# Performance work log

Hardware: AMD Instinct MI355X
Metric: run time of the kernel (lower is better)

The kernel has to match this reference:

```python
import jax, jax.numpy as jnp
import numpy as np

SCALE = 2
GROUPS = 4


def _init_pos(scale, groups, dtype=jnp.float32):
    # h = arange((-s+1)/2, (s-1)/2 + 1) / s
    h = (jnp.arange(scale, dtype=dtype) - (scale - 1) / 2) / scale
    yy, xx = jnp.meshgrid(h, h, indexing='ij')
    pos = jnp.stack([xx, yy], axis=0)              # [2, s, s]
    # torch .repeat(1, groups, 1, 1) tiles along the size-2 dim -> [2*G, s, s]
    return jnp.tile(pos, (groups, 1, 1)).reshape(1, -1, 1, 1)  # [1, 2*G*s*s, 1, 1]


def _pixel_shuffle(x, r):
    B, C, H, W = x.shape
    Co = C // (r * r)
    x = x.reshape(B, Co, r, r, H, W)
    x = x.transpose(0, 1, 4, 2, 5, 3)              # [B, Co, H, r, W, r]
    return x.reshape(B, Co, H * r, W * r)


def _grid_sample_border(img, grid):
    # img: [N, C, H, W]; grid: [N, Ho, Wo, 2] in [-1, 1] (x, y); bilinear,
    # align_corners=False, padding_mode='border' (coords clamped first).
    N, C, H, W = img.shape
    gx, gy = grid[..., 0], grid[..., 1]
    ix = jnp.clip(((gx + 1) * W - 1) * 0.5, 0.0, W - 1)
    iy = jnp.clip(((gy + 1) * H - 1) * 0.5, 0.0, H - 1)
    x0f = jnp.floor(ix); y0f = jnp.floor(iy)
    wx = (ix - x0f)[:, None]                       # [N, 1, Ho, Wo]
    wy = (iy - y0f)[:, None]
    x0 = x0f.astype(jnp.int32); y0 = y0f.astype(jnp.int32)
    x1 = jnp.minimum(x0 + 1, W - 1); y1 = jnp.minimum(y0 + 1, H - 1)

    def gather(im, y, x):                          # im [C,H,W], y/x [Ho,Wo]
        return im[:, y, x]                         # [C, Ho, Wo]
    gv = jax.vmap(gather)

    return ((1 - wy) * ((1 - wx) * gv(img, y0, x0) + wx * gv(img, y0, x1))
            + wy * ((1 - wx) * gv(img, y1, x0) + wx * gv(img, y1, x1)))


def setup_inputs() -> dict:
    key = jax.random.key(0)
    k1, k2 = jax.random.split(key)
    B, C, H, W = 16, 64, 128, 128
    out_ch = 2 * GROUPS * SCALE ** 2               # 32
    x = jax.random.normal(k1, (B, C, H, W), dtype=jnp.float32)
    w_off = jax.random.normal(k2, (out_ch, C), dtype=jnp.float32) * 0.001
    b_off = jnp.zeros((out_ch,), dtype=jnp.float32)
    return {"x": x, "w_off": w_off, "b_off": b_off}


def reference(x, w_off, b_off):
    B, C, H, W = x.shape
    s, G = SCALE, GROUPS
    # 1x1 conv offset, scaled by 0.25, plus fixed sub-pixel init positions
    offset = jnp.einsum('bchw,oc->bohw', x, w_off) + b_off[None, :, None, None]
    offset = offset * 0.25 + _init_pos(s, G, x.dtype)   # [B, 2*G*s*s, H, W]

    off = offset.reshape(B, 2, G * s * s, H, W)
    cx = jnp.arange(W, dtype=x.dtype) + 0.5
    cy = jnp.arange(H, dtype=x.dtype) + 0.5
    yy, xx = jnp.meshgrid(cy, cx, indexing='ij')
    coords = jnp.stack([xx, yy], axis=0)[None, :, None]  # [1, 2, 1, H, W]
    norm = jnp.array([W, H], dtype=x.dtype).reshape(1, 2, 1, 1, 1)
    coords = 2 * (coords + off) / norm - 1               # [B, 2, G*s*s, H, W]

    coords = _pixel_shuffle(coords.reshape(B, 2 * G * s * s, H, W), s)  # [B, 2G, sH, sW]
    grid = coords.reshape(B, 2, G, s * H, s * W)
    grid = grid.transpose(0, 2, 3, 4, 1).reshape(B * G, s * H, s * W, 2)

    out = _grid_sample_border(x.reshape(B * G, C // G, H, W), grid)
    return out.reshape(B, C, s * H, s * W)
```

## Files before the change

### kernel.cpp

```cpp
#include <hip/hip_runtime.h>
#include <hip/hip_fp16.h>


namespace {
constexpr int CC = 64;
constexpr int HH = 128;
constexpr int WW = 128;
constexpr int HW = HH * WW;
constexpr int OW = 2 * WW;
constexpr int OHW = 4 * HW;
constexpr int TH = 8, TW = 32;
constexpr int WS = 36;
constexpr int WPL = 10 * WS;
constexpr int RING = 84;
typedef float vfloat2 __attribute__((ext_vector_type(2)));
}

__global__ __launch_bounds__(256, 2)
void dysample_kernel(const float* __restrict__ x,
                     const float* __restrict__ w_off,
                     const float* __restrict__ b_off,
                     float* __restrict__ out) {
    __shared__ float win[16][WPL];

    const int tid  = threadIdx.x;
    const int wg   = ((int)blockIdx.x & 7) * 128 + ((int)blockIdx.x >> 3);
    const int tile = wg & 63;
    const int b    = wg >> 6;
    const int th0  = (tile >> 2) * TH;
    const int tw0  = (tile & 3) * TW;
    const int ty   = tid >> 5;
    const int tx   = tid & 31;
    const int h    = th0 + ty;
    const int w    = tw0 + tx;

    float xv[64];
    __half2 offs[16];
    {
        float accx[16], accy[16];
#pragma unroll
        for (int j = 0; j < 16; ++j) {
            accx[j] = b_off[j];
            accy[j] = b_off[j + 16];
        }
        const float* xb = x + b * (CC * HW) + h * WW + w;
#pragma unroll
        for (int ch = 0; ch < 4; ++ch) {
#pragma unroll
            for (int c = 0; c < 16; ++c) xv[ch * 16 + c] = xb[(ch * 16 + c) * HW];
#pragma unroll
            for (int j = 0; j < 16; ++j) {
                float ax = accx[j], ay = accy[j];
                const float* wxp = w_off + j * 64 + ch * 16;
                const float* wyp = wxp + 16 * 64;
#pragma unroll
                for (int c = 0; c < 16; ++c) ax = fmaf(xv[ch * 16 + c], wxp[c], ax);
#pragma unroll
                for (int c = 0; c < 16; ++c) ay = fmaf(xv[ch * 16 + c], wyp[c], ay);
                accx[j] = ax; accy[j] = ay;
            }
        }
#pragma unroll
        for (int j = 0; j < 16; ++j) {
            const int g = j >> 2, r1_ = (j >> 1) & 1, r2_ = j & 1;
            const float init = (((g & 1) ? r1_ : r2_) ? 0.25f : -0.25f);
            offs[j] = __floats2half2_rn(fmaf(accx[j], 0.25f, init),
                                        fmaf(accy[j], 0.25f, init));
        }
    }

    int rsrc[6], rdst[6];
#pragma unroll
    for (int i = 0; i < 6; ++i) {
        const int s  = tid + 256 * i;
        const int ci = min(s / RING, 15);
        const int rp = s - ci * RING;
        int ry, rx;
        if (rp < 34)      { ry = 0;       rx = rp; }
        else if (rp < 68) { ry = 9;       rx = rp - 34; }
        else if (rp < 76) { ry = rp - 67; rx = 0; }
        else              { ry = rp - 75; rx = 33; }
        const int gr = min(max(th0 - 1 + ry, 0), HH - 1);
        const int gc = min(max(tw0 - 1 + rx, 0), WW - 1);
        rsrc[i] = ci * HW + gr * WW + gc;
        rdst[i] = ci * WPL + ry * WS + rx;
    }
    const bool v5 = (tid < 16 * RING - 5 * 256);

    const float* xg0 = x + (size_t)b * (CC * HW);
    float ringv[6];
#pragma unroll
    for (int i = 0; i < 6; ++i)
        if (i < 5 || v5) ringv[i] = xg0[rsrc[i]];

    float* const ob = out + (size_t)b * (CC * OHW)
                    + (size_t)(2 * h) * OW + 2 * w;
    const float fw = (float)w, fh = (float)h;

#pragma unroll
    for (int g = 0; g < 4; ++g) {
        __syncthreads();
#pragma unroll
        for (int ci = 0; ci < 16; ++ci)
            win[ci][(ty + 1) * WS + (tx + 1)] = xv[g * 16 + ci];
#pragma unroll
        for (int i = 0; i < 6; ++i)
            if (i < 5 || v5) (&win[0][0])[rdst[i]] = ringv[i];
        __syncthreads();
        if (g < 3) {
#pragma unroll
            for (int i = 0; i < 6; ++i)
                if (i < 5 || v5) ringv[i] = xg0[(g + 1) * (16 * HW) + rsrc[i]];
        }

        float wc[4][3], wr[4][3];
        bool vall = true;
#pragma unroll
        for (int p = 0; p < 4; ++p) {
            const float2 o = __half22float2(offs[g * 4 + p]);
            float ix = ((fw + 0.5f) + o.x) - 0.5f;
            float iy = ((fh + 0.5f) + o.y) - 0.5f;
            ix = fminf(fmaxf(ix, 0.0f), 127.0f);
            iy = fminf(fmaxf(iy, 0.0f), 127.0f);
            const float x0f = floorf(ix), y0f = floorf(iy);
            const float wxf = ix - x0f, wyf = iy - y0f;
            const int sx = (int)x0f - (w - 1);
            const int sy = (int)y0f - (h - 1);
            vall = vall && ((unsigned)sx <= 1u) && ((unsigned)sy <= 1u);
            const bool bx = (sx != 0), by = (sy != 0);
            wc[p][0] = bx ? 0.0f : 1.0f - wxf;
            wc[p][1] = bx ? 1.0f - wxf : wxf;
            wc[p][2] = bx ? wxf : 0.0f;
            wr[p][0] = by ? 0.0f : 1.0f - wyf;
            wr[p][1] = by ? 1.0f - wyf : wyf;
            wr[p][2] = by ? wyf : 0.0f;
        }

        float* const og = ob + (size_t)(g * 16) * OHW;
        if (vall) {
#pragma unroll 2
            for (int c = 0; c < 16; ++c) {
                const float* wp = &win[c][ty * WS + tx];
                const float m0 = wp[0],        m1 = wp[1],          m2 = wp[2];
                const float m3 = wp[WS],       m4 = wp[WS + 1],     m5 = wp[WS + 2];
                const float m6 = wp[2 * WS],   m7 = wp[2 * WS + 1], m8 = wp[2 * WS + 2];
                float res[4];
#pragma unroll
                for (int p = 0; p < 4; ++p) {
                    const float rd0 = fmaf(wc[p][2], m2,
                                      fmaf(wc[p][1], m1, wc[p][0] * m0));
                    const float rd1 = fmaf(wc[p][2], m5,
                                      fmaf(wc[p][1], m4, wc[p][0] * m3));
                    const float rd2 = fmaf(wc[p][2], m8,
                                      fmaf(wc[p][1], m7, wc[p][0] * m6));
                    res[p] = fmaf(wr[p][2], rd2,
                             fmaf(wr[p][1], rd1, wr[p][0] * rd0));
                }
                vfloat2 lo, hi;
                lo.x = res[0]; lo.y = res[1];
                hi.x = res[2]; hi.y = res[3];
                __builtin_nontemporal_store(lo, (vfloat2*)(og + (size_t)c * OHW));
                __builtin_nontemporal_store(hi, (vfloat2*)(og + (size_t)c * OHW + OW));
            }
        } else {
            for (int c = 0; c < 16; ++c) {
                const float* xs = xg0 + (size_t)(g * 16 + c) * HW;
#pragma unroll
                for (int p = 0; p < 4; ++p) {
                    const float2 o = __half22float2(offs[g * 4 + p]);
                    float ix = ((fw + 0.5f) + o.x) - 0.5f;
                    float iy = ((fh + 0.5f) + o.y) - 0.5f;
                    ix = fminf(fmaxf(ix, 0.0f), 127.0f);
                    iy = fminf(fmaxf(iy, 0.0f), 127.0f);
                    const float x0f = floorf(ix), y0f = floorf(iy);
                    const float wxf = ix - x0f, wyf = iy - y0f;
                    const int xa = (int)x0f, ya = (int)y0f;
                    const int xb2 = min(xa + 1, WW - 1);
                    const int yb2 = min(ya + 1, HH - 1);
                    const float v00 = xs[ya * WW + xa],  v01 = xs[ya * WW + xb2];
                    const float v10 = xs[yb2 * WW + xa], v11 = xs[yb2 * WW + xb2];
                    const float t = fmaf(wxf, v01 - v00, v00);
                    const float u = fmaf(wxf, v11 - v10, v10);
                    og[(size_t)c * OHW + (size_t)(p >> 1) * OW + (p & 1)] =
                        fmaf(wyf, u - t, t);
                }
            }
        }
    }
}

extern "C" void kernel_launch(void* const* d_in, const int* in_sizes, int n_in,
                              void* d_out, int out_size, void* d_ws, size_t ws_size,
                              hipStream_t stream) {
    const float* x     = (const float*)d_in[0];
    const float* w_off = (const float*)d_in[1];
    const float* b_off = (const float*)d_in[2];
    float* out = (float*)d_out;
    (void)in_sizes; (void)n_in; (void)out_size; (void)d_ws; (void)ws_size;
    dysample_kernel<<<dim3(1024), dim3(256), 0, stream>>>(x, w_off, b_off, out);
}
```

Before: 388.1 us.

## Retile to full-width row strips with shared offsets and 16-byte output stores

The tile changes from 8x32 pixels to 2 full rows by 128 columns. Border columns are now replicated in place, so the only halo needed is one row above and one below, which removes most of the halo gather logic. Offsets move from per-thread registers into shared memory, so each thread can produce four consecutive output pixels of one output row and write them with a single 16-byte nontemporal store. Launch bounds rise to 3 blocks per SM to raise occupancy, at the cost of more shared memory per block and more register pressure.

```diff
diff --git a/kernel.cpp b/kernel.cpp
--- a/kernel.cpp
+++ b/kernel.cpp
@@ -9,33 +9,37 @@
 constexpr int HW = HH * WW;
 constexpr int OW = 2 * WW;
 constexpr int OHW = 4 * HW;
-constexpr int TH = 8, TW = 32;
-constexpr int WS = 36;
-constexpr int WPL = 10 * WS;
-constexpr int RING = 84;
-typedef float vfloat2 __attribute__((ext_vector_type(2)));
+constexpr int WS2 = 132;
+constexpr int WPL2 = 4 * WS2;
+typedef float vfloat4 __attribute__((ext_vector_type(4)));
 }
 
-__global__ __launch_bounds__(256, 2)
+__global__ __launch_bounds__(256, 3)
 void dysample_kernel(const float* __restrict__ x,
                      const float* __restrict__ w_off,
                      const float* __restrict__ b_off,
                      float* __restrict__ out) {
-    __shared__ float win[16][WPL];
+    __shared__ __half2 offh[16][256];
+    __shared__ float   win[16 * WPL2];
 
     const int tid  = threadIdx.x;
     const int wg   = ((int)blockIdx.x & 7) * 128 + ((int)blockIdx.x >> 3);
     const int tile = wg & 63;
     const int b    = wg >> 6;
-    const int th0  = (tile >> 2) * TH;
-    const int tw0  = (tile & 3) * TW;
-    const int ty   = tid >> 5;
-    const int tx   = tid & 31;
-    const int h    = th0 + ty;
-    const int w    = tw0 + tx;
+    const int th0  = tile * 2;
+    const int ty   = tid >> 7;
+    const int tx   = tid & 127;
+
+    const float* xg0 = x + (size_t)b * (CC * HW);
+
+    const int rrow  = th0 - 1 + ty * 3;
+    const int grow  = min(max(rrow, 0), HH - 1);
+    const int rsrc0 = grow * WW + tx;
+    const int rdst0 = (ty * 3) * WS2 + (tx + 1);
+    const bool e0   = (tx == 0);
+    const bool e127 = (tx == 127);
 
     float xv[64];
-    __half2 offs[16];
     {
         float accx[16], accy[16];
 #pragma unroll
@@ -43,7 +47,7 @@
             accx[j] = b_off[j];
             accy[j] = b_off[j + 16];
         }
-        const float* xb = x + b * (CC * HW) + h * WW + w;
+        const float* xb = xg0 + (th0 + ty) * WW + tx;
 #pragma unroll
         for (int ch = 0; ch < 4; ++ch) {
 #pragma unroll
@@ -60,116 +64,123 @@
                 accx[j] = ax; accy[j] = ay;
             }
         }
+
+        float ringv0[16];
+#pragma unroll
+        for (int c = 0; c < 16; ++c) ringv0[c] = xg0[c * HW + rsrc0];
+
 #pragma unroll
         for (int j = 0; j < 16; ++j) {
             const int g = j >> 2, r1_ = (j >> 1) & 1, r2_ = j & 1;
             const float init = (((g & 1) ? r1_ : r2_) ? 0.25f : -0.25f);
-            offs[j] = __floats2half2_rn(fmaf(accx[j], 0.25f, init),
-                                        fmaf(accy[j], 0.25f, init));
+            offh[j][ty * 128 + tx] = __floats2half2_rn(fmaf(accx[j], 0.25f, init),
+                                                       fmaf(accy[j], 0.25f, init));
+        }
+
+#pragma unroll
+        for (int c = 0; c < 16; ++c) {
+            const int di = c * WPL2 + (1 + ty) * WS2 + (tx + 1);
+            win[di] = xv[c];
+            if (e0)   win[c * WPL2 + (1 + ty) * WS2 + 0]   = xv[c];
+            if (e127) win[c * WPL2 + (1 + ty) * WS2 + 129] = xv[c];
+        }
+#pragma unroll
+        for (int c = 0; c < 16; ++c) {
+            win[c * WPL2 + rdst0] = ringv0[c];
+            if (e0)   win[c * WPL2 + (ty * 3) * WS2 + 0]   = ringv0[c];
+            if (e127) win[c * WPL2 + (ty * 3) * WS2 + 129] = ringv0[c];
         }
     }
-
-    int rsrc[6], rdst[6];
-#pragma unroll
-    for (int i = 0; i < 6; ++i) {
-        const int s  = tid + 256 * i;
-        const int ci = min(s / RING, 15);
-        const int rp = s - ci * RING;
-        int ry, rx;
-        if (rp < 34)      { ry = 0;       rx = rp; }
-        else if (rp < 68) { ry = 9;       rx = rp - 34; }
-        else if (rp < 76) { ry = rp - 67; rx = 0; }
-        else              { ry = rp - 75; rx = 33; }
-        const int gr = min(max(th0 - 1 + ry, 0), HH - 1);
-        const int gc = min(max(tw0 - 1 + rx, 0), WW - 1);
-        rsrc[i] = ci * HW + gr * WW + gc;
-        rdst[i] = ci * WPL + ry * WS + rx;
-    }
-    const bool v5 = (tid < 16 * RING - 5 * 256);
-
-    const float* xg0 = x + (size_t)b * (CC * HW);
-    float ringv[6];
-#pragma unroll
-    for (int i = 0; i < 6; ++i)
-        if (i < 5 || v5) ringv[i] = xg0[rsrc[i]];
-
-    float* const ob = out + (size_t)b * (CC * OHW)
-                    + (size_t)(2 * h) * OW + 2 * w;
-    const float fw = (float)w, fh = (float)h;
-
+    __syncthreads();
+
+    const int oy  = tid >> 6;
+    const int x4  = tid & 63;
+    const int hl2 = oy >> 1;
+    const int r1  = oy & 1;
+    const int jb  = 2 * x4;
+    const float fhh = (float)(th0 + hl2);
+    float* const obase = out + (size_t)b * (CC * OHW)
+                       + (size_t)(2 * th0 + oy) * OW + 4 * x4;
+
+    float ringv[16];
 #pragma unroll
     for (int g = 0; g < 4; ++g) {
-        __syncthreads();
-#pragma unroll
-        for (int ci = 0; ci < 16; ++ci)
-            win[ci][(ty + 1) * WS + (tx + 1)] = xv[g * 16 + ci];
-#pragma unroll
-        for (int i = 0; i < 6; ++i)
-            if (i < 5 || v5) (&win[0][0])[rdst[i]] = ringv[i];
-        __syncthreads();
         if (g < 3) {
 #pragma unroll
-            for (int i = 0; i < 6; ++i)
-                if (i < 5 || v5) ringv[i] = xg0[(g + 1) * (16 * HW) + rsrc[i]];
-        }
-
-        float wc[4][3], wr[4][3];
+            for (int c = 0; c < 16; ++c)
+                ringv[c] = xg0[((g + 1) * 16 + c) * HW + rsrc0];
+        }
+
+        float wcq[4][3], wrq[4][3];
         bool vall = true;
 #pragma unroll
-        for (int p = 0; p < 4; ++p) {
-            const float2 o = __half22float2(offs[g * 4 + p]);
-            float ix = ((fw + 0.5f) + o.x) - 0.5f;
-            float iy = ((fh + 0.5f) + o.y) - 0.5f;
+        for (int k = 0; k < 4; ++k) {
+            const int q  = g * 4 + (r1 << 1) + (k & 1);
+            const int wl = jb + (k >> 1);
+            const float2 o = __half22float2(offh[q][hl2 * 128 + wl]);
+            float ix = (((float)wl + 0.5f) + o.x) - 0.5f;
+            float iy = ((fhh + 0.5f) + o.y) - 0.5f;
             ix = fminf(fmaxf(ix, 0.0f), 127.0f);
             iy = fminf(fmaxf(iy, 0.0f), 127.0f);
             const float x0f = floorf(ix), y0f = floorf(iy);
             const float wxf = ix - x0f, wyf = iy - y0f;
-            const int sx = (int)x0f - (w - 1);
-            const int sy = (int)y0f - (h - 1);
+            const int sx = (int)x0f - (wl - 1);
+            const int sy = (int)y0f - (th0 + hl2 - 1);
             vall = vall && ((unsigned)sx <= 1u) && ((unsigned)sy <= 1u);
             const bool bx = (sx != 0), by = (sy != 0);
-            wc[p][0] = bx ? 0.0f : 1.0f - wxf;
-            wc[p][1] = bx ? 1.0f - wxf : wxf;
-            wc[p][2] = bx ? wxf : 0.0f;
-            wr[p][0] = by ? 0.0f : 1.0f - wyf;
-            wr[p][1] = by ? 1.0f - wyf : wyf;
-            wr[p][2] = by ? wyf : 0.0f;
-        }
-
-        float* const og = ob + (size_t)(g * 16) * OHW;
+            wcq[k][0] = bx ? 0.0f : 1.0f - wxf;
+            wcq[k][1] = bx ? 1.0f - wxf : wxf;
+            wcq[k][2] = bx ? wxf : 0.0f;
+            wrq[k][0] = by ? 0.0f : 1.0f - wyf;
+            wrq[k][1] = by ? 1.0f - wyf : wyf;
+            wrq[k][2] = by ? wyf : 0.0f;
+        }
+
         if (vall) {
-#pragma unroll 2
-            for (int c = 0; c < 16; ++c) {
-                const float* wp = &win[c][ty * WS + tx];
-                const float m0 = wp[0],        m1 = wp[1],          m2 = wp[2];
-                const float m3 = wp[WS],       m4 = wp[WS + 1],     m5 = wp[WS + 2];
-                const float m6 = wp[2 * WS],   m7 = wp[2 * WS + 1], m8 = wp[2 * WS + 2];
-                float res[4];
-#pragma unroll
-                for (int p = 0; p < 4; ++p) {
-                    const float rd0 = fmaf(wc[p][2], m2,
-                                      fmaf(wc[p][1], m1, wc[p][0] * m0));
-                    const float rd1 = fmaf(wc[p][2], m5,
-                                      fmaf(wc[p][1], m4, wc[p][0] * m3));
-                    const float rd2 = fmaf(wc[p][2], m8,
-                                      fmaf(wc[p][1], m7, wc[p][0] * m6));
-                    res[p] = fmaf(wr[p][2], rd2,
-                             fmaf(wr[p][1], rd1, wr[p][0] * rd0));
+#pragma unroll
+            for (int c = 0; c < 16; ++c) {
+                const float* wp = &win[c * WPL2 + hl2 * WS2 + jb];
+                const float t00 = wp[0],           t01 = wp[1];
+                const float t02 = wp[2],           t03 = wp[3];
+                const float t10 = wp[WS2],         t11 = wp[WS2 + 1];
+                const float t12 = wp[WS2 + 2],     t13 = wp[WS2 + 3];
+                const float t20 = wp[2 * WS2],     t21 = wp[2 * WS2 + 1];
+                const float t22 = wp[2 * WS2 + 2], t23 = wp[2 * WS2 + 3];
+                vfloat4 res;
+#pragma unroll
+                for (int k = 0; k < 4; ++k) {
+                    const float a0 = (k >> 1) ? t01 : t00;
+                    const float a1 = (k >> 1) ? t02 : t01;
+                    const float a2 = (k >> 1) ? t03 : t02;
+                    const float b0 = (k >> 1) ? t11 : t10;
+                    const float b1 = (k >> 1) ? t12 : t11;
+                    const float b2 = (k >> 1) ? t13 : t12;
+                    const float c0 = (k >> 1) ? t21 : t20;
+                    const float c1 = (k >> 1) ? t22 : t21;
+                    const float c2 = (k >> 1) ? t23 : t22;
+                    const float rd0 = fmaf(wcq[k][2], a2,
+                                      fmaf(wcq[k][1], a1, wcq[k][0] * a0));
+                    const float rd1 = fmaf(wcq[k][2], b2,
+                                      fmaf(wcq[k][1], b1, wcq[k][0] * b0));
+                    const float rd2 = fmaf(wcq[k][2], c2,
+                                      fmaf(wcq[k][1], c1, wcq[k][0] * c0));
+                    res[k] = fmaf(wrq[k][2], rd2,
+                             fmaf(wrq[k][1], rd1, wrq[k][0] * rd0));
                 }
-                vfloat2 lo, hi;
-                lo.x = res[0]; lo.y = res[1];
-                hi.x = res[2]; hi.y = res[3];
-                __builtin_nontemporal_store(lo, (vfloat2*)(og + (size_t)c * OHW));
-                __builtin_nontemporal_store(hi, (vfloat2*)(og + (size_t)c * OHW + OW));
+                __builtin_nontemporal_store(
+                    res, (vfloat4*)(obase + (size_t)(g * 16 + c) * OHW));
             }
         } else {
             for (int c = 0; c < 16; ++c) {
                 const float* xs = xg0 + (size_t)(g * 16 + c) * HW;
-#pragma unroll
-                for (int p = 0; p < 4; ++p) {
-                    const float2 o = __half22float2(offs[g * 4 + p]);
-                    float ix = ((fw + 0.5f) + o.x) - 0.5f;
-                    float iy = ((fh + 0.5f) + o.y) - 0.5f;
+                float* og = obase + (size_t)(g * 16 + c) * OHW;
+#pragma unroll
+                for (int k = 0; k < 4; ++k) {
+                    const int q  = g * 4 + (r1 << 1) + (k & 1);
+                    const int wl = jb + (k >> 1);
+                    const float2 o = __half22float2(offh[q][hl2 * 128 + wl]);
+                    float ix = (((float)wl + 0.5f) + o.x) - 0.5f;
+                    float iy = ((fhh + 0.5f) + o.y) - 0.5f;
                     ix = fminf(fmaxf(ix, 0.0f), 127.0f);
                     iy = fminf(fmaxf(iy, 0.0f), 127.0f);
                     const float x0f = floorf(ix), y0f = floorf(iy);
@@ -181,10 +192,27 @@
                     const float v10 = xs[yb2 * WW + xa], v11 = xs[yb2 * WW + xb2];
                     const float t = fmaf(wxf, v01 - v00, v00);
                     const float u = fmaf(wxf, v11 - v10, v10);
-                    og[(size_t)c * OHW + (size_t)(p >> 1) * OW + (p & 1)] =
-                        fmaf(wyf, u - t, t);
+                    og[k] = fmaf(wyf, u - t, t);
                 }
             }
+        }
+
+        if (g < 3) {
+            __syncthreads();
+#pragma unroll
+            for (int c = 0; c < 16; ++c) {
+                const float v = xv[(g + 1) * 16 + c];
+                win[c * WPL2 + (1 + ty) * WS2 + (tx + 1)] = v;
+                if (e0)   win[c * WPL2 + (1 + ty) * WS2 + 0]   = v;
+                if (e127) win[c * WPL2 + (1 + ty) * WS2 + 129] = v;
+            }
+#pragma unroll
+            for (int c = 0; c < 16; ++c) {
+                win[c * WPL2 + rdst0] = ringv[c];
+                if (e0)   win[c * WPL2 + (ty * 3) * WS2 + 0]   = ringv[c];
+                if (e127) win[c * WPL2 + (ty * 3) * WS2 + 129] = ringv[c];
+            }
+            __syncthreads();
         }
     }
 }
```

After: 368.6 us. -5.0%, faster.
